# Kernel tuning notes

Hardware: AMD Instinct MI355X
Metric: run time of the kernel (lower is better)

The kernel has to match this reference:

```python
import jax, jax.numpy as jnp
import numpy as np

D_MODEL = 1024
NUM_HEADS = 16
D_K = D_MODEL // NUM_HEADS
SCALE = D_K ** 0.5


def setup_inputs() -> dict:
    key = jax.random.key(0)
    k1, k2, k3, k4, k5 = jax.random.split(key, 5)
    B, T = 4, 2048
    x = jax.random.normal(k1, (B, T, D_MODEL), dtype=jnp.float32)
    # torch nn.Linear: y = x @ W.T + b ; store W in (in, out) layout for jax
    s = 1.0 / np.sqrt(D_MODEL)
    w_qkv = jax.random.uniform(k2, (D_MODEL, 3 * D_MODEL), jnp.float32, -s, s)
    b_qkv = jax.random.uniform(k3, (3 * D_MODEL,), jnp.float32, -s, s)
    w_out = jax.random.uniform(k4, (D_MODEL, D_MODEL), jnp.float32, -s, s)
    b_out = jax.random.uniform(k5, (D_MODEL,), jnp.float32, -s, s)
    return {"x": x, "w_qkv": w_qkv, "b_qkv": b_qkv, "w_out": w_out, "b_out": b_out}


def reference(x, w_qkv, b_qkv, w_out, b_out):
    B, T, D = x.shape
    qkv = x @ w_qkv + b_qkv  # (B, T, 3D)
    q, k, v = jnp.split(qkv, 3, axis=-1)

    def split_heads(t):
        return t.reshape(B, T, NUM_HEADS, D_K).transpose(0, 2, 1, 3)  # (B,H,T,d_k)

    q, k, v = split_heads(q), split_heads(k), split_heads(v)
    scores = jnp.einsum("bhtd,bhsd->bhts", q, k) / SCALE  # (B,H,T,T)
    attn = jax.nn.softmax(scores, axis=-1)
    ctx = jnp.einsum("bhts,bhsd->bhtd", attn, v)  # (B,H,T,d_k)
    ctx = ctx.transpose(0, 2, 1, 3).reshape(B, T, D)
    y = ctx @ w_out + b_out
    return y
```

## Files before the change

kernel.cpp:

```cpp
#include <hip/hip_runtime.h>
#include <hip/hip_bf16.h>


using v8bf  = __attribute__((ext_vector_type(8))) __bf16;
using f32x4 = __attribute__((ext_vector_type(4))) float;
using f32x16 = __attribute__((ext_vector_type(16))) float;
typedef unsigned int uv2 __attribute__((ext_vector_type(2)));

__device__ __forceinline__ unsigned short f2bf(float f) {
  union { float f; unsigned int u; } v; v.f = f;
  unsigned int u = v.u;
  u += 0x7FFFu + ((u >> 16) & 1u);
  return (unsigned short)(u >> 16);
}

#if __has_builtin(__builtin_amdgcn_cvt_pk_bf16_f32)
__device__ __forceinline__ unsigned int pack2bf(float a, float b) {
  typedef __bf16 bf16x2 __attribute__((ext_vector_type(2)));
  bf16x2 r = __builtin_amdgcn_cvt_pk_bf16_f32(a, b);
  return __builtin_bit_cast(unsigned int, r);
}
#else
__device__ __forceinline__ unsigned int pack2bf(float a, float b) {
  return (unsigned int)f2bf(a) | ((unsigned int)f2bf(b) << 16);
}
#endif

__device__ __forceinline__ void async16(const void* g, void* l) {
  __builtin_amdgcn_global_load_lds(
      (__attribute__((address_space(1))) void*)g,
      (__attribute__((address_space(3))) void*)l, 16, 0, 0);
}

__global__ __launch_bounds__(256) void prepass(const float* __restrict__ x,
                                               unsigned short* __restrict__ XB,
                                               const float* __restrict__ wq,
                                               unsigned short* __restrict__ WQT,
                                               const float* __restrict__ wo,
                                               unsigned short* __restrict__ WOT) {
  const int bid = blockIdx.x;
  if (bid < 8192) {
    const int i = (bid * 256 + threadIdx.x) * 4;
    float4 v = *(const float4*)(x + i);
    ushort4 o;
    o.x = f2bf(v.x); o.y = f2bf(v.y); o.z = f2bf(v.z); o.w = f2bf(v.w);
    *(ushort4*)(XB + i) = o;
  } else {
    const float* in; unsigned short* out; int N, tb;
    if (bid < 8960) { in = wq; out = WQT; N = 3072; tb = bid - 8192; }
    else            { in = wo; out = WOT; N = 1024; tb = bid - 8960; }
    __shared__ unsigned short tile[64][65];
    const int k0 = (tb & 15) * 64, n0 = (tb >> 4) * 64;
    for (int i = threadIdx.x; i < 4096; i += 256) {
      int r = i >> 6, c = i & 63;
      tile[r][c] = f2bf(in[(size_t)(k0 + r) * N + n0 + c]);
    }
    __syncthreads();
    for (int i = threadIdx.x; i < 4096; i += 256) {
      int r = i >> 6, c = i & 63;
      out[(size_t)(n0 + r) * 1024 + k0 + c] = tile[c][r];
    }
  }
}

__device__ __forceinline__ void gemm128(const unsigned short* __restrict__ A,
                                        const unsigned short* __restrict__ Bt,
                                        int m0, int n0,
                                        unsigned short* As, unsigned short* Bs,
                                        f32x4 acc[4][4]) {
  const int tid = threadIdx.x;
  const int w = tid >> 6, lane = tid & 63, quad = lane >> 4, l16 = lane & 15;
  const int wm = (w >> 1) * 64, wn = (w & 1) * 64;

  const int srow = w * 32 + (lane >> 3);
  const int cg = (lane & 7) ^ (lane >> 3);
  const size_t a_g = (size_t)(m0 + srow) * 1024 + cg * 8;
  const size_t b_g = (size_t)(n0 + srow) * 1024 + cg * 8;
  const int lds_off = srow * 64 + (lane & 7) * 8;

  const int l7 = l16 & 7;
  const int a_rd0 = (wm + l16) * 128 + ((quad ^ l7) << 4);
  const int a_rd1 = (wm + l16) * 128 + (((4 + quad) ^ l7) << 4);
  const int b_rd0 = (wn + l16) * 128 + ((quad ^ l7) << 4);
  const int b_rd1 = (wn + l16) * 128 + (((4 + quad) ^ l7) << 4);

  for (int k0 = 0; k0 < 1024; k0 += 64) {
#pragma unroll
    for (int j = 0; j < 4; j++) {
      async16(A + a_g + (size_t)j * 8192 + k0, As + lds_off + j * 512);
      async16(Bt + b_g + (size_t)j * 8192 + k0, Bs + lds_off + j * 512);
    }
    __syncthreads();
#pragma unroll
    for (int ks = 0; ks < 2; ks++) {
      v8bf af[4], bfr[4];
#pragma unroll
      for (int i = 0; i < 4; i++) {
        af[i]  = *(const v8bf*)((const char*)As + (ks ? a_rd1 : a_rd0) + i * 2048);
        bfr[i] = *(const v8bf*)((const char*)Bs + (ks ? b_rd1 : b_rd0) + i * 2048);
      }
#pragma unroll
      for (int i = 0; i < 4; i++)
#pragma unroll
        for (int jn = 0; jn < 4; jn++)
          acc[i][jn] = __builtin_amdgcn_mfma_f32_16x16x32_bf16(af[i], bfr[jn], acc[i][jn], 0, 0, 0);
    }
    __syncthreads();
  }
}

__global__ __launch_bounds__(256) void qkv_gemm(const unsigned short* __restrict__ xb,
                                                const unsigned short* __restrict__ wt,
                                                const float* __restrict__ bias,
                                                unsigned short* __restrict__ Q,
                                                unsigned short* __restrict__ K,
                                                unsigned short* __restrict__ VT) {
  __shared__ __align__(16) unsigned char pool[128 * 136 * 2];
  unsigned short* As = (unsigned short*)pool;
  unsigned short* Bs = (unsigned short*)(pool + 16384);
  unsigned short* Tr = (unsigned short*)pool;

  f32x4 acc[4][4];
#pragma unroll
  for (int i = 0; i < 4; i++)
#pragma unroll
    for (int j = 0; j < 4; j++) acc[i][j] = (f32x4){0.f, 0.f, 0.f, 0.f};

  const int m0 = blockIdx.x * 128, n0 = blockIdx.y * 128;
  gemm128(xb, wt, m0, n0, As, Bs, acc);

  const int tid = threadIdx.x;
  const int w = tid >> 6, lane = tid & 63, quad = lane >> 4, l16 = lane & 15;
  const int wm = (w >> 1) * 64, wn = (w & 1) * 64;
  const int seg = n0 >> 10;

  if (seg < 2) {
    const float sc = (seg == 0) ? 0.18033688011112042f : 1.0f;
    unsigned short* dst = (seg == 0) ? Q : K;
#pragma unroll
    for (int jn = 0; jn < 4; jn++) {
      const int n = n0 + wn + jn * 16 + l16;
      const float bv = bias[n];
      const int nn = n & 1023, h = nn >> 6, d = nn & 63;
#pragma unroll
      for (int i = 0; i < 4; i++) {
#pragma unroll
        for (int r = 0; r < 4; r++) {
          const int m = m0 + wm + i * 16 + quad * 4 + r;
          const int b_ = m >> 11, t = m & 2047;
          dst[(((size_t)(b_ * 16 + h)) * 2048 + t) * 64 + d] =
              f2bf((acc[i][jn][r] + bv) * sc);
        }
      }
    }
  } else {
    const int TP = 136;
#pragma unroll
    for (int jn = 0; jn < 4; jn++) {
      const int nl = wn + jn * 16 + l16;
      const float bv = bias[n0 + nl];
#pragma unroll
      for (int i = 0; i < 4; i++) {
        const int ml = wm + i * 16 + quad * 4;
        ushort4 v4;
        v4.x = f2bf(acc[i][jn][0] + bv);
        v4.y = f2bf(acc[i][jn][1] + bv);
        v4.z = f2bf(acc[i][jn][2] + bv);
        v4.w = f2bf(acc[i][jn][3] + bv);
        *(ushort4*)&Tr[nl * TP + ml] = v4;
      }
    }
    __syncthreads();
    const int rl = tid >> 1, cb = (tid & 1) * 64;
    const int h0 = (n0 & 1023) >> 6;
    const int h = h0 + (rl >> 6), d = rl & 63;
    const int b_ = m0 >> 11, t = m0 & 2047;
    unsigned short* dst = VT + (((size_t)(b_ * 16 + h)) * 64 + d) * 2048 + t + cb;
    const unsigned short* src = &Tr[rl * TP + cb];
#pragma unroll
    for (int c = 0; c < 8; c++)
      *(uint4*)(dst + c * 8) = *(const uint4*)(src + c * 8);
  }
}

__global__ __launch_bounds__(256, 2) void flash_attn(const unsigned short* __restrict__ Q,
                                                     const unsigned short* __restrict__ K,
                                                     const unsigned short* __restrict__ VT,
                                                     unsigned short* __restrict__ ctx) {
  const int bh    = blockIdx.x;
  const int qtile = blockIdx.y;
  const int tid = threadIdx.x;
  const int w = tid >> 6, lane = tid & 63, hi = lane >> 5, l32 = lane & 31;
  const int q0 = qtile * 256;

  const unsigned short* Qb = Q  + (size_t)bh * 2048 * 64;
  const unsigned short* Kb = K  + (size_t)bh * 2048 * 64;
  const unsigned short* Vb = VT + (size_t)bh * 64 * 2048;

  __shared__ __align__(16) unsigned short Ks[3 * 4096];
  __shared__ __align__(16) unsigned short Vs[3 * 4096];

  const int sr = w * 8 + (lane >> 3);
  const int cg = (lane & 7) ^ ((lane >> 3) & 7);
  const int lds_off = sr * 64 + (lane & 7) * 8;

  v8bf qf[2][4];
#pragma unroll
  for (int qt = 0; qt < 2; qt++) {
    const int qrow = q0 + w * 64 + qt * 32 + l32;
#pragma unroll
    for (int kc = 0; kc < 4; kc++)
      qf[qt][kc] = *(const v8bf*)(Qb + (size_t)qrow * 64 + kc * 16 + hi * 8);
  }

  f32x16 o[2][2];
  f32x16 st[2][2];
  float l_[2] = {0.f, 0.f};
#pragma unroll
  for (int qt = 0; qt < 2; qt++)
#pragma unroll
    for (int mt = 0; mt < 2; mt++)
#pragma unroll
      for (int r = 0; r < 16; r++) o[qt][mt][r] = 0.f;

  f32x16 fz;
#pragma unroll
  for (int r = 0; r < 16; r++) fz[r] = 0.f;

  auto stage = [&](int buf, int s0) {
    unsigned short* Kd = Ks + buf * 4096;
    unsigned short* Vd = Vs + buf * 4096;
#pragma unroll
    for (int j = 0; j < 2; j++) {
      async16(Kb + (size_t)(s0 + sr + j * 32) * 64 + cg * 8, Kd + lds_off + j * 2048);
      async16(Vb + (size_t)(sr + j * 32) * 2048 + s0 + cg * 8, Vd + lds_off + j * 2048);
    }
  };

  const int l7 = l32 & 7;

  auto computeS = [&](const unsigned short* Kc) {
#pragma unroll
    for (int sf = 0; sf < 2; sf++) {
      v8bf ak[4];
#pragma unroll
      for (int kc = 0; kc < 4; kc++)
        ak[kc] = *(const v8bf*)((const char*)Kc +
                   (sf * 32 + l32) * 128 + (((2 * kc + hi) ^ l7) << 4));
#pragma unroll
      for (int qt = 0; qt < 2; qt++) {
        f32x16 s = __builtin_amdgcn_mfma_f32_32x32x16_bf16(ak[0], qf[qt][0], fz, 0, 0, 0);
#pragma unroll
        for (int kc = 1; kc < 4; kc++)
          s = __builtin_amdgcn_mfma_f32_32x32x16_bf16(ak[kc], qf[qt][kc], s, 0, 0, 0);
        st[qt][sf] = s;
      }
    }
  };

  auto softmax_pack = [&](uint2 pk[2][2][4]) {
#pragma unroll
    for (int qt = 0; qt < 2; qt++) {
      float a = 0.f;
#pragma unroll
      for (int sf = 0; sf < 2; sf++)
#pragma unroll
        for (int r = 0; r < 16; r++) {
          const float pv = __builtin_amdgcn_exp2f(st[qt][sf][r]);
          st[qt][sf][r] = pv;
          a += pv;
        }
      l_[qt] += a;
#pragma unroll
      for (int sf = 0; sf < 2; sf++)
#pragma unroll
        for (int g = 0; g < 4; g++) {
          pk[qt][sf][g].x = pack2bf(st[qt][sf][g * 4 + 0], st[qt][sf][g * 4 + 1]);
          pk[qt][sf][g].y = pack2bf(st[qt][sf][g * 4 + 2], st[qt][sf][g * 4 + 3]);
        }
    }
  };

  auto pv = [&](const unsigned short* Vc, uint2 pk[2][2][4]) {
    v8bf vf[2][4];
#pragma unroll
    for (int mt = 0; mt < 2; mt++)
#pragma unroll
      for (int kc = 0; kc < 4; kc++)
        vf[mt][kc] = *(const v8bf*)((const char*)Vc +
                       (mt * 32 + l32) * 128 + (((2 * kc + hi) ^ l7) << 4));
#pragma unroll
    for (int qt = 0; qt < 2; qt++) {
#pragma unroll
      for (int kc = 0; kc < 4; kc++) {
        const int sf = kc >> 1, c2 = (kc & 1) * 2;
        const uint2 olo = pk[qt][sf][c2];
        const uint2 ohi = pk[qt][sf][c2 + 1];
        uint4 u;
#if __has_builtin(__builtin_amdgcn_permlane32_swap)
        uv2 rx = __builtin_amdgcn_permlane32_swap(olo.x, ohi.x, false, false);
        uv2 ry = __builtin_amdgcn_permlane32_swap(olo.y, ohi.y, false, false);
        u.x = rx[0]; u.y = ry[0]; u.z = rx[1]; u.w = ry[1];
#else
        uint2 send, recv;
        send.x = hi ? olo.x : ohi.x;
        send.y = hi ? olo.y : ohi.y;
        recv.x = __shfl_xor(send.x, 32, 64);
        recv.y = __shfl_xor(send.y, 32, 64);
        u.x = hi ? recv.x : olo.x;
        u.y = hi ? recv.y : olo.y;
        u.z = hi ? ohi.x : recv.x;
        u.w = hi ? ohi.y : recv.y;
#endif
        const v8bf pf = __builtin_bit_cast(v8bf, u);
#pragma unroll
        for (int mt = 0; mt < 2; mt++)
          o[qt][mt] = __builtin_amdgcn_mfma_f32_32x32x16_bf16(vf[mt][kc], pf, o[qt][mt], 0, 0, 0);
      }
    }
  };

  stage(0, 0);
  __syncthreads();
  stage(1, 64);
  computeS(Ks);

  int cs = 1, cp = 0, cn = 2;
  for (int it = 1; it < 32; ++it) {
    __syncthreads();
    if (it < 31) stage(cn, (it + 1) * 64);
    uint2 pk[2][2][4];
    softmax_pack(pk);
    computeS(Ks + cs * 4096);
    pv(Vs + cp * 4096, pk);
    const int t = cp; cp = cs; cs = cn; cn = t;
  }
  {
    uint2 pk[2][2][4];
    softmax_pack(pk);
    pv(Vs + cp * 4096, pk);
  }

  const int b_ = bh >> 4, h = bh & 15;
#pragma unroll
  for (int qt = 0; qt < 2; qt++) {
    float lt = l_[qt];
    lt += __shfl_xor(lt, 32, 64);
    const float inv = 1.0f / lt;
    const int t = q0 + w * 64 + qt * 32 + l32;
    unsigned short* cr = ctx + ((size_t)(b_ * 2048 + t)) * 1024 + h * 64;
#pragma unroll
    for (int mt = 0; mt < 2; mt++)
#pragma unroll
      for (int g = 0; g < 4; g++) {
        uint2 pkv;
        pkv.x = pack2bf(o[qt][mt][g * 4 + 0] * inv, o[qt][mt][g * 4 + 1] * inv);
        pkv.y = pack2bf(o[qt][mt][g * 4 + 2] * inv, o[qt][mt][g * 4 + 3] * inv);
        *(uint2*)(cr + mt * 32 + g * 8 + hi * 4) = pkv;
      }
  }
}

__global__ __launch_bounds__(256) void out_gemm(const unsigned short* __restrict__ ctx,
                                                const unsigned short* __restrict__ wt,
                                                const float* __restrict__ bias,
                                                float* __restrict__ out) {
  __shared__ __align__(16) unsigned short As[128 * 64];
  __shared__ __align__(16) unsigned short Bs[128 * 64];
  f32x4 acc[4][4];
#pragma unroll
  for (int i = 0; i < 4; i++)
#pragma unroll
    for (int j = 0; j < 4; j++) acc[i][j] = (f32x4){0.f, 0.f, 0.f, 0.f};

  const int m0 = blockIdx.x * 128, n0 = blockIdx.y * 128;
  gemm128(ctx, wt, m0, n0, As, Bs, acc);

  const int tid = threadIdx.x;
  const int w = tid >> 6, lane = tid & 63, quad = lane >> 4, l16 = lane & 15;
  const int wm = (w >> 1) * 64, wn = (w & 1) * 64;
#pragma unroll
  for (int jn = 0; jn < 4; jn++) {
    const int n = n0 + wn + jn * 16 + l16;
    const float bv = bias[n];
#pragma unroll
    for (int i = 0; i < 4; i++) {
#pragma unroll
      for (int r = 0; r < 4; r++) {
        const int m = m0 + wm + i * 16 + quad * 4 + r;
        out[(size_t)m * 1024 + n] = acc[i][jn][r] + bv;
      }
    }
  }
}

extern "C" void kernel_launch(void* const* d_in, const int* in_sizes, int n_in,
                              void* d_out, int out_size, void* d_ws, size_t ws_size,
                              hipStream_t stream) {
  const float* x     = (const float*)d_in[0];
  const float* w_qkv = (const float*)d_in[1];
  const float* b_qkv = (const float*)d_in[2];
  const float* w_out = (const float*)d_in[3];
  const float* b_out = (const float*)d_in[4];
  float* out = (float*)d_out;

  char* ws = (char*)d_ws;
  unsigned short* XB  = (unsigned short*)(ws + 0);
  unsigned short* WQT = (unsigned short*)(ws + 16777216);
  unsigned short* WOT = (unsigned short*)(ws + 23068672);
  unsigned short* Qp  = (unsigned short*)(ws + 25165824);
  unsigned short* Kp  = (unsigned short*)(ws + 41943040);
  unsigned short* VTp = (unsigned short*)(ws + 58720256);
  unsigned short* CTX = (unsigned short*)(ws + 75497472);

  prepass<<<9216, 256, 0, stream>>>(x, XB, w_qkv, WQT, w_out, WOT);
  qkv_gemm<<<dim3(64, 24), 256, 0, stream>>>(XB, WQT, b_qkv, Qp, Kp, VTp);
  flash_attn<<<dim3(64, 8), 256, 0, stream>>>(Qp, Kp, VTp, CTX);
  out_gemm<<<dim3(64, 8), 256, 0, stream>>>(CTX, WOT, b_out, out);
}
```

Baseline: 262.2 us.

## Rewrite QKV GEMM as 256x256 tile, 8-wave, async double-buffered pipeline

The QKV projection GEMM moves from a 128x128 tile with 4 waves to a 256x256 tile with 8 waves. It uses async global-to-LDS loads into XOR-swizzled double buffers, staged loads interleaved with the MFMA quarters, s_setprio around the compute, and a block-id swizzle for L2 locality. The V-transpose epilogue is split into two phases so it fits the staging buffer. This is meant to raise arithmetic intensity and overlap memory with compute, at the cost of 128KB of LDS per block and heavier register pressure.

New measurement: 276.8 us. 1.06x slower.

```diff
diff --git a/kernel.cpp b/kernel.cpp
--- a/kernel.cpp
+++ b/kernel.cpp
@@ -109,77 +109,155 @@
   }
 }
 
-__global__ __launch_bounds__(256) void qkv_gemm(const unsigned short* __restrict__ xb,
-                                                const unsigned short* __restrict__ wt,
-                                                const float* __restrict__ bias,
-                                                unsigned short* __restrict__ Q,
-                                                unsigned short* __restrict__ K,
-                                                unsigned short* __restrict__ VT) {
-  __shared__ __align__(16) unsigned char pool[128 * 136 * 2];
-  unsigned short* As = (unsigned short*)pool;
-  unsigned short* Bs = (unsigned short*)(pool + 16384);
-  unsigned short* Tr = (unsigned short*)pool;
-
-  f32x4 acc[4][4];
-#pragma unroll
-  for (int i = 0; i < 4; i++)
+__global__ __launch_bounds__(512, 2) void qkv_gemm(const unsigned short* __restrict__ xb,
+                                                   const unsigned short* __restrict__ wt,
+                                                   const float* __restrict__ bias,
+                                                   unsigned short* __restrict__ Q,
+                                                   unsigned short* __restrict__ K,
+                                                   unsigned short* __restrict__ VT) {
+  __shared__ __align__(16) unsigned char pool[131072];
+  unsigned short* AsL = (unsigned short*)pool;
+  unsigned short* BsL = (unsigned short*)(pool + 65536);
+  unsigned short* Tr  = (unsigned short*)pool;
+
+  const int tid = threadIdx.x;
+  const int wid = tid >> 6, lane = tid & 63;
+  const int quad = lane >> 4, l16 = lane & 15, l7 = l16 & 7;
+  const int wm = (wid >> 2) * 128, wn = (wid & 3) * 64;
+
+  const int id = blockIdx.x;
+  const int swz = (id & 7) * 48 + (id >> 3);
+  const int mt = swz & 31, nt = swz >> 5;
+  const int m0 = mt * 256, n0 = nt * 256;
+
+  const int cg = (lane & 7) ^ (lane >> 3);
+
+  f32x4 acc[8][4];
+#pragma unroll
+  for (int i = 0; i < 8; i++)
 #pragma unroll
     for (int j = 0; j < 4; j++) acc[i][j] = (f32x4){0.f, 0.f, 0.f, 0.f};
 
-  const int m0 = blockIdx.x * 128, n0 = blockIdx.y * 128;
-  gemm128(xb, wt, m0, n0, As, Bs, acc);
-
-  const int tid = threadIdx.x;
-  const int w = tid >> 6, lane = tid & 63, quad = lane >> 4, l16 = lane & 15;
-  const int wm = (w >> 1) * 64, wn = (w & 1) * 64;
+  auto stageHalf = [&](int isB, int h, int kt) {
+    const unsigned short* G = isB ? wt : xb;
+    const int rbase = (isB ? n0 : m0) + h * 128;
+    unsigned short* dst = (isB ? BsL : AsL) + (kt & 1) * 16384 + h * 8192
+                          + wid * 512 + lane * 8;
+#pragma unroll
+    for (int j = 0; j < 2; j++)
+      async16(G + (size_t)(rbase + j * 64 + wid * 8 + (lane >> 3)) * 1024
+                + kt * 64 + cg * 8,
+              dst + j * 4096);
+  };
+
+  stageHalf(1, 0, 0); stageHalf(1, 1, 0);
+  stageHalf(0, 0, 0); stageHalf(0, 1, 0);
+  stageHalf(1, 0, 1); stageHalf(1, 1, 1);
+  asm volatile("s_waitcnt vmcnt(4)" ::: "memory");
+  __builtin_amdgcn_s_barrier();
+
+  const int rB = wn & 64;
+  v8bf bfr[4][2];
+
+  for (int kt = 0; kt < 16; ++kt) {
+    const unsigned short* Ah = AsL + (kt & 1) * 16384 + (wid >> 2) * 8192;
+    const unsigned short* Bh = BsL + (kt & 1) * 16384 + ((wid >> 1) & 1) * 8192;
+#pragma unroll
+    for (int q = 0; q < 4; ++q) {
+      if (q == 0) {
+        if (kt == 15)     asm volatile("s_waitcnt vmcnt(0)" ::: "memory");
+        else if (kt > 0)  asm volatile("s_waitcnt vmcnt(4)" ::: "memory");
+      }
+      if (q == 0) {
+#pragma unroll
+        for (int j = 0; j < 4; j++)
+#pragma unroll
+          for (int ks = 0; ks < 2; ks++)
+            bfr[j][ks] = *(const v8bf*)((const char*)Bh +
+                (rB + j * 16 + l16) * 128 + (((ks * 4 + quad) ^ l7) << 4));
+      }
+      v8bf af[2][2];
+#pragma unroll
+      for (int i = 0; i < 2; i++)
+#pragma unroll
+        for (int ks = 0; ks < 2; ks++)
+          af[i][ks] = *(const v8bf*)((const char*)Ah +
+              (q * 32 + i * 16 + l16) * 128 + (((ks * 4 + quad) ^ l7) << 4));
+      if (q <= 1) { if (kt < 15) stageHalf(0, q, kt + 1); }
+      else        { if (kt < 14) stageHalf(1, q - 2, kt + 2); }
+      if (q == 0) asm volatile("s_waitcnt lgkmcnt(8)" ::: "memory");
+      __builtin_amdgcn_s_barrier();
+      asm volatile("s_waitcnt lgkmcnt(0)" ::: "memory");
+      __builtin_amdgcn_s_setprio(1);
+#pragma unroll
+      for (int i = 0; i < 2; i++)
+#pragma unroll
+        for (int ks = 0; ks < 2; ks++)
+#pragma unroll
+          for (int j = 0; j < 4; j++)
+            acc[q * 2 + i][j] = __builtin_amdgcn_mfma_f32_16x16x32_bf16(
+                af[i][ks], bfr[j][ks], acc[q * 2 + i][j], 0, 0, 0);
+      __builtin_amdgcn_s_setprio(0);
+      __builtin_amdgcn_s_barrier();
+    }
+  }
+
   const int seg = n0 >> 10;
-
   if (seg < 2) {
     const float sc = (seg == 0) ? 0.18033688011112042f : 1.0f;
     unsigned short* dst = (seg == 0) ? Q : K;
 #pragma unroll
-    for (int jn = 0; jn < 4; jn++) {
-      const int n = n0 + wn + jn * 16 + l16;
+    for (int j = 0; j < 4; j++) {
+      const int n = n0 + wn + j * 16 + l16;
       const float bv = bias[n];
       const int nn = n & 1023, h = nn >> 6, d = nn & 63;
 #pragma unroll
-      for (int i = 0; i < 4; i++) {
+      for (int i = 0; i < 8; i++) {
 #pragma unroll
         for (int r = 0; r < 4; r++) {
           const int m = m0 + wm + i * 16 + quad * 4 + r;
           const int b_ = m >> 11, t = m & 2047;
           dst[(((size_t)(b_ * 16 + h)) * 2048 + t) * 64 + d] =
-              f2bf((acc[i][jn][r] + bv) * sc);
+              f2bf((acc[i][j][r] + bv) * sc);
         }
       }
     }
   } else {
     const int TP = 136;
 #pragma unroll
-    for (int jn = 0; jn < 4; jn++) {
-      const int nl = wn + jn * 16 + l16;
-      const float bv = bias[n0 + nl];
-#pragma unroll
-      for (int i = 0; i < 4; i++) {
-        const int ml = wm + i * 16 + quad * 4;
-        ushort4 v4;
-        v4.x = f2bf(acc[i][jn][0] + bv);
-        v4.y = f2bf(acc[i][jn][1] + bv);
-        v4.z = f2bf(acc[i][jn][2] + bv);
-        v4.w = f2bf(acc[i][jn][3] + bv);
-        *(ushort4*)&Tr[nl * TP + ml] = v4;
-      }
-    }
-    __syncthreads();
-    const int rl = tid >> 1, cb = (tid & 1) * 64;
-    const int h0 = (n0 & 1023) >> 6;
-    const int h = h0 + (rl >> 6), d = rl & 63;
-    const int b_ = m0 >> 11, t = m0 & 2047;
-    unsigned short* dst = VT + (((size_t)(b_ * 16 + h)) * 64 + d) * 2048 + t + cb;
-    const unsigned short* src = &Tr[rl * TP + cb];
-#pragma unroll
-    for (int c = 0; c < 8; c++)
-      *(uint4*)(dst + c * 8) = *(const uint4*)(src + c * 8);
+    for (int ph = 0; ph < 2; ph++) {
+      if ((wid >> 2) == ph) {
+#pragma unroll
+        for (int j = 0; j < 4; j++) {
+          const int nl = wn + j * 16 + l16;
+          const float bv = bias[n0 + nl];
+#pragma unroll
+          for (int i = 0; i < 8; i++) {
+            const int ml = i * 16 + quad * 4;
+            ushort4 v4;
+            v4.x = f2bf(acc[i][j][0] + bv);
+            v4.y = f2bf(acc[i][j][1] + bv);
+            v4.z = f2bf(acc[i][j][2] + bv);
+            v4.w = f2bf(acc[i][j][3] + bv);
+            *(ushort4*)&Tr[nl * TP + ml] = v4;
+          }
+        }
+      }
+      __syncthreads();
+      {
+        const int rl = tid >> 1, cb = (tid & 1) * 64;
+        const int h0 = (n0 & 1023) >> 6;
+        const int h = h0 + (rl >> 6), d = rl & 63;
+        const int b_ = m0 >> 11;
+        const int t0 = (m0 & 2047) + ph * 128 + cb;
+        unsigned short* dstp = VT + (((size_t)(b_ * 16 + h)) * 64 + d) * 2048 + t0;
+        const unsigned short* src = &Tr[rl * TP + cb];
+#pragma unroll
+        for (int c = 0; c < 8; c++)
+          *(uint4*)(dstp + c * 8) = *(const uint4*)(src + c * 8);
+      }
+      __syncthreads();
+    }
   }
 }
 
@@ -414,7 +492,7 @@
   unsigned short* CTX = (unsigned short*)(ws + 75497472);
 
   prepass<<<9216, 256, 0, stream>>>(x, XB, w_qkv, WQT, w_out, WOT);
-  qkv_gemm<<<dim3(64, 24), 256, 0, stream>>>(XB, WQT, b_qkv, Qp, Kp, VTp);
+  qkv_gemm<<<384, 512, 0, stream>>>(XB, WQT, b_qkv, Qp, Kp, VTp);
   flash_attn<<<dim3(64, 8), 256, 0, stream>>>(Qp, Kp, VTp, CTX);
   out_gemm<<<dim3(64, 8), 256, 0, stream>>>(CTX, WOT, b_out, out);
 }
```
